# Kernel tuning notes

Measured on AMD Instinct MI355X. Metric: run time of the kernel, lower is better.

The kernel has to match this reference:

```python
import jax, jax.numpy as jnp
import numpy as np

N, E, F_IN, HID, HEADS = 10000, 160000, 70, 256, 4
NEG_SLOPE = 0.2


def setup_inputs() -> dict:
    key = jax.random.key(0)
    ks = jax.random.split(key, 12)
    p = lambda k, shape: jax.random.normal(k, shape, jnp.float32) * 0.05
    return dict(
        node_features=jax.random.normal(ks[0], (N, F_IN), jnp.float32),
        edge_index=jax.random.randint(ks[1], (2, E), 0, N),
        edge_attr=jax.random.normal(ks[2], (E, 4), jnp.float32),
        W1=p(ks[3], (F_IN, HEADS * HID)),
        att_src1=p(ks[4], (HEADS, HID)),
        att_dst1=p(ks[5], (HEADS, HID)),
        b1=jnp.zeros((HEADS * HID,), jnp.float32),
        W2=p(ks[6], (HEADS * HID, HID)),
        att_src2=p(ks[7], (1, HID)),
        att_dst2=p(ks[8], (1, HID)),
        b2=jnp.zeros((HID,), jnp.float32),
        Wv1=p(ks[9], (HID, 128)),
        bv1=jnp.zeros((128,), jnp.float32),
        Wv2=p(ks[10], (128, 1)),
        bv2=jnp.zeros((1,), jnp.float32),
    )


def _gat_layer(x, src, dst, W, a_src, a_dst, b, heads, ch, concat):
    """PyG GATConv (edge_dim=None, add_self_loops already applied to src/dst)."""
    n = x.shape[0]
    h = (x @ W).reshape(n, heads, ch)                      # [N,H,C]
    a_s = (h * a_src).sum(-1)                              # [N,H]
    a_d = (h * a_dst).sum(-1)                              # [N,H]
    e = jax.nn.leaky_relu(a_s[src] + a_d[dst], NEG_SLOPE)  # [E,H]
    # segment softmax over incoming edges of each destination node
    m = jax.ops.segment_max(e, dst, num_segments=n)        # [N,H]
    m = jnp.where(jnp.isfinite(m), m, 0.0)
    ex = jnp.exp(e - m[dst])
    denom = jax.ops.segment_sum(ex, dst, num_segments=n)[dst] + 1e-16
    alpha = ex / denom                                     # [E,H]
    out = jax.ops.segment_sum(h[src] * alpha[..., None], dst, num_segments=n)  # [N,H,C]
    out = out.reshape(n, heads * ch) if concat else out.mean(axis=1)
    return out + b


def reference(node_features, edge_index, edge_attr, W1, att_src1, att_dst1, b1,
              W2, att_src2, att_dst2, b2, Wv1, bv1, Wv2, bv2):
    # edge_attr is ignored: GATConv built without edge_dim has lin_edge=None.
    n = node_features.shape[0]
    loops = jnp.arange(n, dtype=edge_index.dtype)
    src = jnp.concatenate([edge_index[0], loops])
    dst = jnp.concatenate([edge_index[1], loops])
    x = jax.nn.relu(_gat_layer(node_features, src, dst, W1, att_src1, att_dst1, b1, HEADS, HID, True))
    x = jax.nn.relu(_gat_layer(x, src, dst, W2, att_src2, att_dst2, b2, 1, HID, False))
    pooled = x.mean(axis=0, keepdims=True)                 # [1,HID]
    hmid = jax.nn.gelu(pooled @ Wv1 + bv1, approximate=False)
    return hmid @ Wv2 + bv2                                # [1,1]
```

## Files before the change

### kernel.cpp

```cpp
#include <hip/hip_runtime.h>
#include <math.h>

#define NN   10000
#define NE   160000
#define NET  (NE + NN)
#define FIN  70
#define HIDC 256
#define NH   4
#define D1   1024
#define SLOPE 0.2f
#define KL1  96
#define NPB  32
#define BCAP 64

typedef float f32x4 __attribute__((ext_vector_type(4)));
typedef short bf16x8 __attribute__((ext_vector_type(8)));
typedef unsigned short u16x4 __attribute__((ext_vector_type(4)));

__device__ __forceinline__ unsigned short f32_to_bf16(float f) {
    unsigned int u = __float_as_uint(f);
    unsigned int r = u + 0x7fffu + ((u >> 16) & 1u);
    return (unsigned short)(r >> 16);
}
__device__ __forceinline__ float bf16_to_f32(unsigned short h) {
    return __uint_as_float(((unsigned int)h) << 16);
}
__device__ __forceinline__ float leaky(float e) { return (e > 0.f) ? e : SLOPE * e; }

__device__ __forceinline__ void cp16(const unsigned short* g, unsigned short* l) {
    __builtin_amdgcn_global_load_lds((const __attribute__((address_space(1))) unsigned int*)g,
                                     (__attribute__((address_space(3))) unsigned int*)l,
                                     16, 0, 0);
}

__global__ __launch_bounds__(256) void k_prep(const float* __restrict__ W2,
                                              unsigned short* __restrict__ W2t,
                                              const float* __restrict__ W1,
                                              unsigned short* __restrict__ W1t,
                                              const float* __restrict__ asrc,
                                              const float* __restrict__ adst,
                                              const float* __restrict__ x,
                                              unsigned short* __restrict__ xb,
                                              const int* __restrict__ ei,
                                              int* __restrict__ cnt,
                                              int* __restrict__ ssrc,
                                              float* __restrict__ asn,
                                              float* __restrict__ adn) {
    __shared__ __align__(16) char smem[20480];
    int b = blockIdx.x, t = threadIdx.x;
    int lane = t & 63, wave = t >> 6;
    if (b < 64) {
        unsigned short (*tl)[68] = (unsigned short (*)[68])smem;
        int kk0 = (b >> 2) * 64, n0 = (b & 3) * 64;
        for (int i = t; i < 64 * 64; i += 256) {
            int nl = i & 63, kl = i >> 6;
            tl[nl][kl] = f32_to_bf16(W2[(size_t)(kk0 + kl) * HIDC + n0 + nl]);
        }
        __syncthreads();
        for (int i = t; i < 64 * 64; i += 256) {
            int kl = i & 63, nl = i >> 6;
            W2t[(size_t)(n0 + nl) * 1024 + kk0 + kl] = tl[nl][kl];
        }
    } else if (b < 80) {
        unsigned short (*tl)[97] = (unsigned short (*)[97])smem;
        int r0 = (b - 64) * 64;
        for (int i = t; i < 64 * 96; i += 256) {
            int rl = i & 63, kk = i >> 6;
            float w = (kk < FIN) ? W1[(size_t)kk * D1 + r0 + rl] : 0.f;
            tl[rl][kk] = f32_to_bf16(w);
        }
        __syncthreads();
        for (int i = t; i < 64 * 96; i += 256) {
            int kk = i % 96, rl = i / 96;
            W1t[(size_t)(r0 + rl) * KL1 + kk] = tl[rl][kk];
        }
    } else if (b < 120) {
        size_t base = (size_t)(b - 80) * 17500;
        for (int v = t; v < 4375; v += 256) {
            float4 xv = *(const float4*)&x[base + v * 4];
            u16x4 o;
            o[0] = f32_to_bf16(xv.x); o[1] = f32_to_bf16(xv.y);
            o[2] = f32_to_bf16(xv.z); o[3] = f32_to_bf16(xv.w);
            *(u16x4*)&xb[base + v * 4] = o;
        }
    } else if (b < 785) {
        int e = (b - 120) * 256 + t;
        if (e < NET) {
            int src, dst;
            if (e < NE) { src = ei[e]; dst = ei[NE + e]; }
            else        { src = e - NE; dst = src; }
            int pos = atomicAdd(&cnt[dst], 1);
            if (pos < BCAP) ssrc[dst * BCAP + pos] = src;
        }
    } else {
        int n0 = (b - 785) * 64;
        float (*xs)[71] = (float (*)[71])smem;
        float* lws = (float*)(smem + 64 * 71 * 4);
        float* lwd = lws + NH * FIN;
        for (int i = t; i < 64 * FIN; i += 256) {
            int r = i / FIN, k = i % FIN;
            int n = n0 + r;
            xs[r][k] = (n < NN) ? x[(size_t)n * FIN + k] : 0.f;
        }
        float ar[16], dr[16];
#pragma unroll
        for (int q = 0; q < 4; q++) {
            float4 av = *(const float4*)&asrc[lane * 16 + q * 4];
            float4 dv = *(const float4*)&adst[lane * 16 + q * 4];
            ar[q*4+0]=av.x; ar[q*4+1]=av.y; ar[q*4+2]=av.z; ar[q*4+3]=av.w;
            dr[q*4+0]=dv.x; dr[q*4+1]=dv.y; dr[q*4+2]=dv.z; dr[q*4+3]=dv.w;
        }
        for (int k = wave; k < FIN; k += 4) {
            const float* row = W1 + (size_t)k * D1 + lane * 16;
            float s = 0.f, dd = 0.f;
#pragma unroll
            for (int q = 0; q < 4; q++) {
                float4 wv = *(const float4*)(row + q * 4);
                s  += wv.x*ar[q*4] + wv.y*ar[q*4+1] + wv.z*ar[q*4+2] + wv.w*ar[q*4+3];
                dd += wv.x*dr[q*4] + wv.y*dr[q*4+1] + wv.z*dr[q*4+2] + wv.w*dr[q*4+3];
            }
#pragma unroll
            for (int off = 1; off < 16; off <<= 1) { s += __shfl_xor(s, off); dd += __shfl_xor(dd, off); }
            if ((lane & 15) == 0) { int h = lane >> 4; lws[h * FIN + k] = s; lwd[h * FIN + k] = dd; }
        }
        __syncthreads();
        if (t < 64) {
            int n = n0 + t;
            if (n < NN) {
                float a[NH] = {}, d2[NH] = {};
                for (int k = 0; k < FIN; k++) {
                    float xv = xs[t][k];
#pragma unroll
                    for (int h = 0; h < NH; h++) {
                        a[h]  += xv * lws[h * FIN + k];
                        d2[h] += xv * lwd[h * FIN + k];
                    }
                }
#pragma unroll
                for (int h = 0; h < NH; h++) { asn[n*NH+h] = a[h]; adn[n*NH+h] = d2[h]; }
            }
        }
    }
}

__global__ __launch_bounds__(256) void k_sm_aggX(const int* __restrict__ cnt,
                                                 const int* __restrict__ ssrc,
                                                 const float* __restrict__ as,
                                                 const float* __restrict__ ad,
                                                 const unsigned short* __restrict__ xb,
                                                 unsigned short* __restrict__ aggXhi) {
    int t = threadIdx.x, lane = t & 63, wave = t >> 6;
    int d = blockIdx.x * 4 + wave;
    int n = cnt[d]; if (n > BCAP) n = BCAP;
    float4 adv = *(const float4*)&ad[d * NH];
    bool v0 = lane < n;
    int s0 = 0;
    float e0[NH];
    if (v0) {
        s0 = ssrc[d * BCAP + lane];
        float4 a4 = *(const float4*)&as[s0 * NH];
        e0[0] = leaky(a4.x + adv.x); e0[1] = leaky(a4.y + adv.y);
        e0[2] = leaky(a4.z + adv.z); e0[3] = leaky(a4.w + adv.w);
    } else { e0[0] = e0[1] = e0[2] = e0[3] = -1e30f; }
    float m[NH] = {e0[0], e0[1], e0[2], e0[3]};
#pragma unroll
    for (int h = 0; h < NH; h++)
        for (int off = 32; off > 0; off >>= 1)
            m[h] = fmaxf(m[h], __shfl_xor(m[h], off));
    float sum[NH];
#pragma unroll
    for (int h = 0; h < NH; h++) sum[h] = v0 ? expf(e0[h] - m[h]) : 0.f;
#pragma unroll
    for (int h = 0; h < NH; h++)
        for (int off = 32; off > 0; off >>= 1)
            sum[h] += __shfl_xor(sum[h], off);
    __shared__ float al4[4][64][4];
    __shared__ int   sid[4][64];
    if (v0) {
        sid[wave][lane] = s0;
#pragma unroll
        for (int h = 0; h < NH; h++) al4[wave][lane][h] = expf(e0[h] - m[h]) / (sum[h] + 1e-16f);
    }
    __syncthreads();
    float ac[NH][2] = {};
#pragma unroll 4
    for (int j = 0; j < n; j++) {
        int s = sid[wave][j];
        float4 al = *(const float4*)al4[wave][j];
        float xv0 = bf16_to_f32(xb[(size_t)s * FIN + lane]);
        float xv1 = (lane < FIN - 64) ? bf16_to_f32(xb[(size_t)s * FIN + 64 + lane]) : 0.f;
        ac[0][0] += al.x * xv0; ac[0][1] += al.x * xv1;
        ac[1][0] += al.y * xv0; ac[1][1] += al.y * xv1;
        ac[2][0] += al.z * xv0; ac[2][1] += al.z * xv1;
        ac[3][0] += al.w * xv0; ac[3][1] += al.w * xv1;
    }
#pragma unroll
    for (int h = 0; h < NH; h++) {
        size_t base = ((size_t)d * NH + h) * KL1;
        aggXhi[base + lane] = f32_to_bf16(ac[h][0]);
        if (lane < 32) {
            float v1 = (lane < FIN - 64) ? ac[h][1] : 0.f;
            aggXhi[base + 64 + lane] = f32_to_bf16(v1);
        }
    }
}

__global__ __launch_bounds__(256) void k_gemm_l1(const unsigned short* __restrict__ aggXhi,
                                                 const unsigned short* __restrict__ W1t,
                                                 const float* __restrict__ b1,
                                                 unsigned short* __restrict__ x2hi) {
    __shared__ unsigned short As[128 * 96];
    __shared__ unsigned short Bs[128 * 96];
    int t = threadIdx.x;
    int n0 = blockIdx.x * 128;
    int cb = blockIdx.y * 128;
    int h  = blockIdx.z;
    int lane = t & 63, wave = t >> 6, quad = lane >> 4, l16 = lane & 15;
    int wr = (wave & 1) * 64, wc = (wave >> 1) * 64;
#pragma unroll
    for (int q = 0; q < 6; q++) {
        int g = q * 256 + t;
        int row = g / 12, gr = g % 12;
        int ra = n0 + row; if (ra >= NN) ra = NN - 1;
        cp16(aggXhi + ((size_t)ra * NH + h) * KL1 + gr * 8, As + g * 8);
        cp16(W1t + (size_t)(h * 256 + cb + row) * KL1 + gr * 8, Bs + g * 8);
    }
    __syncthreads();
    f32x4 acc[4][4] = {};
#pragma unroll
    for (int kc = 0; kc < 3; kc++) {
        bf16x8 af[4], bf[4];
#pragma unroll
        for (int i = 0; i < 4; i++) af[i] = *(const bf16x8*)&As[(wr + i * 16 + l16) * KL1 + kc * 32 + quad * 8];
#pragma unroll
        for (int j = 0; j < 4; j++) bf[j] = *(const bf16x8*)&Bs[(wc + j * 16 + l16) * KL1 + kc * 32 + quad * 8];
#pragma unroll
        for (int i = 0; i < 4; i++)
#pragma unroll
            for (int j = 0; j < 4; j++)
                acc[i][j] = __builtin_amdgcn_mfma_f32_16x16x32_bf16(af[i], bf[j], acc[i][j], 0, 0, 0);
    }
#pragma unroll
    for (int i = 0; i < 4; i++)
#pragma unroll
        for (int j = 0; j < 4; j++) {
            int colg = h * 256 + cb + wc + j * 16 + l16;
            float bb = b1[colg];
#pragma unroll
            for (int reg = 0; reg < 4; reg++) {
                int r = n0 + wr + i * 16 + quad * 4 + reg;
                if (r >= NN) continue;
                float v = fmaxf(acc[i][j][reg] + bb, 0.f);
                x2hi[(size_t)r * D1 + colg] = f32_to_bf16(v);
            }
        }
}

__global__ __launch_bounds__(256) void k_gemm2(const unsigned short* __restrict__ x2hi,
                                               const unsigned short* __restrict__ W2t,
                                               const float* __restrict__ asrc,
                                               const float* __restrict__ adst,
                                               unsigned short* __restrict__ h2bf,
                                               float* __restrict__ as2,
                                               float* __restrict__ ad2) {
    __shared__ unsigned short As[64 * 128];
    __shared__ unsigned short Bs[64 * 128];
    int t = threadIdx.x;
    int n0 = blockIdx.x * 64;
    int cb = blockIdx.y * 64;
    int lane = t & 63, wave = t >> 6, quad = lane >> 4, l16 = lane & 15;
    int wr = (wave & 1) * 32, wc = (wave >> 1) * 32;
    const unsigned short* ga[4];
    unsigned short* la[4];
    const unsigned short* gb[4];
    unsigned short* lb[4];
#pragma unroll
    for (int q = 0; q < 4; q++) {
        int g = q * 256 + t;
        int row = g >> 4, gr = g & 15;
        int ra = n0 + row; if (ra >= NN) ra = NN - 1;
        ga[q] = x2hi + (size_t)ra * D1 + gr * 8;
        la[q] = As + g * 8;
        gb[q] = W2t + (size_t)(cb + row) * 1024 + gr * 8;
        lb[q] = Bs + g * 8;
    }
    f32x4 acc[2][2] = {};
    for (int kc = 0; kc < 8; kc++) {
#pragma unroll
        for (int q = 0; q < 4; q++) {
            cp16(ga[q] + kc * 128, la[q]);
            cp16(gb[q] + kc * 128, lb[q]);
        }
        __syncthreads();
#pragma unroll
        for (int ks = 0; ks < 4; ks++) {
            bf16x8 af[2], bf[2];
#pragma unroll
            for (int i = 0; i < 2; i++) af[i] = *(const bf16x8*)&As[(wr + i * 16 + l16) * 128 + ks * 32 + quad * 8];
#pragma unroll
            for (int j = 0; j < 2; j++) bf[j] = *(const bf16x8*)&Bs[(wc + j * 16 + l16) * 128 + ks * 32 + quad * 8];
#pragma unroll
            for (int i = 0; i < 2; i++)
#pragma unroll
                for (int j = 0; j < 2; j++)
                    acc[i][j] = __builtin_amdgcn_mfma_f32_16x16x32_bf16(af[i], bf[j], acc[i][j], 0, 0, 0);
        }
        __syncthreads();
    }
    float a2[2], d2[2];
#pragma unroll
    for (int j = 0; j < 2; j++) {
        int c = cb + wc + j * 16 + l16;
        a2[j] = asrc[c];
        d2[j] = adst[c];
    }
    float asp[2][4] = {}, adp[2][4] = {};
#pragma unroll
    for (int i = 0; i < 2; i++)
#pragma unroll
        for (int j = 0; j < 2; j++) {
            int c = cb + wc + j * 16 + l16;
#pragma unroll
            for (int reg = 0; reg < 4; reg++) {
                int r = n0 + wr + i * 16 + quad * 4 + reg;
                float v = acc[i][j][reg];
                if (r < NN) h2bf[(size_t)r * HIDC + c] = f32_to_bf16(v);
                asp[i][reg] += v * a2[j];
                adp[i][reg] += v * d2[j];
            }
        }
#pragma unroll
    for (int mask = 1; mask < 16; mask <<= 1)
#pragma unroll
        for (int i = 0; i < 2; i++)
#pragma unroll
            for (int reg = 0; reg < 4; reg++) {
                asp[i][reg] += __shfl_xor(asp[i][reg], mask);
                adp[i][reg] += __shfl_xor(adp[i][reg], mask);
            }
    if (l16 == 0) {
#pragma unroll
        for (int i = 0; i < 2; i++)
#pragma unroll
            for (int reg = 0; reg < 4; reg++) {
                int r = n0 + wr + i * 16 + quad * 4 + reg;
                if (r < NN) {
                    atomicAdd(&as2[r], asp[i][reg]);
                    atomicAdd(&ad2[r], adp[i][reg]);
                }
            }
    }
}

__global__ __launch_bounds__(256) void k_sm_aggr2(const int* __restrict__ cnt,
                                                  const int* __restrict__ ssrc,
                                                  const float* __restrict__ as,
                                                  const float* __restrict__ ad,
                                                  const unsigned short* __restrict__ h2bf,
                                                  const float* __restrict__ b,
                                                  float* __restrict__ pooled32) {
    int t = threadIdx.x, lane = t & 63, wave = t >> 6;
    int d = blockIdx.x * 4 + wave;
    int n = cnt[d]; if (n > BCAP) n = BCAP;
    float adv = ad[d];
    bool v0 = lane < n;
    int s0 = v0 ? ssrc[d * BCAP + lane] : 0;
    float e0 = v0 ? leaky(as[s0] + adv) : -1e30f;
    float m = e0;
    for (int off = 32; off > 0; off >>= 1) m = fmaxf(m, __shfl_xor(m, off));
    float ex = v0 ? expf(e0 - m) : 0.f;
    float sum = ex;
    for (int off = 32; off > 0; off >>= 1) sum += __shfl_xor(sum, off);
    float al0 = ex * (1.0f / (sum + 1e-16f));
    float a0 = 0.f, a1 = 0.f, a2v = 0.f, a3 = 0.f;
#pragma unroll 4
    for (int j = 0; j < n; j++) {
        float alj = __shfl(al0, j);
        int   sj  = __shfl(s0, j);
        u16x4 hv = *(const u16x4*)&h2bf[(size_t)sj * HIDC + lane * 4];
        a0  += alj * bf16_to_f32(hv[0]);
        a1  += alj * bf16_to_f32(hv[1]);
        a2v += alj * bf16_to_f32(hv[2]);
        a3  += alj * bf16_to_f32(hv[3]);
    }
    float4 bb = *(const float4*)&b[lane * 4];
    __shared__ float sacc[4 * 256];
    *(float4*)&sacc[wave * 256 + lane * 4] = make_float4(fmaxf(a0 + bb.x, 0.f),
                                                         fmaxf(a1 + bb.y, 0.f),
                                                         fmaxf(a2v + bb.z, 0.f),
                                                         fmaxf(a3 + bb.w, 0.f));
    __syncthreads();
    float s = sacc[t] + sacc[256 + t] + sacc[512 + t] + sacc[768 + t];
    atomicAdd(&pooled32[(blockIdx.x & (NPB - 1)) * HIDC + t], s);
}

__global__ __launch_bounds__(128) void k_mlp(const float* __restrict__ pooled32,
                                             const float* __restrict__ Wv1,
                                             const float* __restrict__ bv1,
                                             const float* __restrict__ Wv2,
                                             const float* __restrict__ bv2,
                                             float* __restrict__ out) {
    int j = threadIdx.x;
    __shared__ float ps[256];
    for (int c = j; c < HIDC; c += 128) {
        float s = 0.f;
        for (int bkt = 0; bkt < NPB; bkt++) s += pooled32[bkt * HIDC + c];
        ps[c] = s;
    }
    __syncthreads();
    float s = bv1[j];
    const float invn = 1.0f / (float)NN;
    for (int c = 0; c < HIDC; c++)
        s += (ps[c] * invn) * Wv1[c * 128 + j];
    float g = 0.5f * s * (1.0f + erff(s * 0.70710678118654752f));
    float v = g * Wv2[j];
    __shared__ float red[128];
    red[j] = v;
    __syncthreads();
    for (int off = 64; off > 0; off >>= 1) {
        if (j < off) red[j] += red[j + off];
        __syncthreads();
    }
    if (j == 0) out[0] = red[0] + bv2[0];
}

extern "C" void kernel_launch(void* const* d_in, const int* in_sizes, int n_in,
                              void* d_out, int out_size, void* d_ws, size_t ws_size,
                              hipStream_t stream) {
    const float* x_in  = (const float*)d_in[0];
    const int*   ei    = (const int*)d_in[1];
    const float* W1    = (const float*)d_in[3];
    const float* asrc1 = (const float*)d_in[4];
    const float* adst1 = (const float*)d_in[5];
    const float* b1    = (const float*)d_in[6];
    const float* W2    = (const float*)d_in[7];
    const float* asrc2 = (const float*)d_in[8];
    const float* adst2 = (const float*)d_in[9];
    const float* b2    = (const float*)d_in[10];
    const float* Wv1   = (const float*)d_in[11];
    const float* bv1   = (const float*)d_in[12];
    const float* Wv2   = (const float*)d_in[13];
    const float* bv2   = (const float*)d_in[14];
    float* out = (float*)d_out;

    char* w = (char*)d_ws;
    auto alloc = [&](size_t bytes) { char* p = w; w += (bytes + 255) & ~(size_t)255; return p; };
    unsigned short* x2hi   = (unsigned short*)alloc(2ull * NN * D1);
    unsigned short* aggXhi = (unsigned short*)alloc(2ull * NN * NH * KL1);
    unsigned short* h2bf = (unsigned short*)alloc(2ull * NN * HIDC);
    unsigned short* xb   = (unsigned short*)alloc(2ull * NN * FIN);
    unsigned short* W2t  = (unsigned short*)alloc(2ull * 256 * 1024);
    unsigned short* W1t  = (unsigned short*)alloc(2ull * NH * 256 * KL1);
    float* as1    = (float*)alloc(sizeof(float) * NN * NH);
    float* ad1    = (float*)alloc(sizeof(float) * NN * NH);
    int*   ssrc   = (int*)alloc(sizeof(int) * NN * BCAP);
    size_t zbytes = (size_t)NN * 4 + NPB * HIDC * 4 + NN * 4 + NN * 4;
    char*  zbase  = alloc(zbytes);
    int*   cnt      = (int*)zbase;
    float* pooled32 = (float*)(zbase + NN * 4);
    float* as2      = (float*)(zbase + NN * 4 + NPB * HIDC * 4);
    float* ad2      = (float*)(zbase + NN * 4 + NPB * HIDC * 4 + NN * 4);

    hipMemsetAsync(zbase, 0, zbytes, stream);

    k_prep<<<64 + 16 + 40 + 665 + 157, 256, 0, stream>>>(
        W2, W2t, W1, W1t, asrc1, adst1, x_in, xb, ei, cnt, ssrc, as1, ad1);

    k_sm_aggX<<<NN / 4, 256, 0, stream>>>(cnt, ssrc, as1, ad1, xb, aggXhi);
    {
        dim3 g((NN + 127) / 128, 2, NH);
        k_gemm_l1<<<g, 256, 0, stream>>>(aggXhi, W1t, b1, x2hi);
    }

    {
        dim3 g((NN + 63) / 64, 4);
        k_gemm2<<<g, 256, 0, stream>>>(x2hi, W2t, asrc2, adst2, h2bf, as2, ad2);
    }

    k_sm_aggr2<<<NN / 4, 256, 0, stream>>>(cnt, ssrc, as2, ad2, h2bf, b2, pooled32);

    k_mlp<<<1, 128, 0, stream>>>(pooled32, Wv1, bv1, Wv2, bv2, out);
}
```

Baseline: 207.8 us.

## Fuse layer-1 GEMM and layer-2 GEMM into one kernel keeping x2 in LDS

Merges the layer-1 projection GEMM (aggX times W1 with bias and ReLU) and the layer-2 GEMM (x2 times W2 with attention dot products) into one kernel that processes 32 nodes per block. The intermediate 1024-wide x2 activation stays in LDS with an XOR swizzle instead of a 20MB bf16 round trip through global memory. It also removes one launch. In exchange, W1 and W2 fragments are read straight from global or L2 per block with no LDS staging, and there are only 313 blocks with small 32-row tiles, which may hurt occupancy and the MFMA feed rate.

```diff
diff --git a/kernel.cpp b/kernel.cpp
--- a/kernel.cpp
+++ b/kernel.cpp
@@ -26,12 +26,6 @@
     return __uint_as_float(((unsigned int)h) << 16);
 }
 __device__ __forceinline__ float leaky(float e) { return (e > 0.f) ? e : SLOPE * e; }
-
-__device__ __forceinline__ void cp16(const unsigned short* g, unsigned short* l) {
-    __builtin_amdgcn_global_load_lds((const __attribute__((address_space(1))) unsigned int*)g,
-                                     (__attribute__((address_space(3))) unsigned int*)l,
-                                     16, 0, 0);
-}
 
 __global__ __launch_bounds__(256) void k_prep(const float* __restrict__ W2,
                                               unsigned short* __restrict__ W2t,
@@ -205,112 +199,91 @@
     }
 }
 
-__global__ __launch_bounds__(256) void k_gemm_l1(const unsigned short* __restrict__ aggXhi,
-                                                 const unsigned short* __restrict__ W1t,
-                                                 const float* __restrict__ b1,
-                                                 unsigned short* __restrict__ x2hi) {
-    __shared__ unsigned short As[128 * 96];
-    __shared__ unsigned short Bs[128 * 96];
+__global__ __launch_bounds__(256) void k_gemm12(const unsigned short* __restrict__ aggXhi,
+                                                const unsigned short* __restrict__ W1t,
+                                                const float* __restrict__ b1,
+                                                const unsigned short* __restrict__ W2t,
+                                                const float* __restrict__ asrc,
+                                                const float* __restrict__ adst,
+                                                unsigned short* __restrict__ h2bf,
+                                                float* __restrict__ as2,
+                                                float* __restrict__ ad2) {
+    __shared__ unsigned short aggXs[32 * 392];
+    __shared__ unsigned short x2s[32 * 512];
     int t = threadIdx.x;
-    int n0 = blockIdx.x * 128;
-    int cb = blockIdx.y * 128;
-    int h  = blockIdx.z;
+    int n0 = blockIdx.x * 32;
     int lane = t & 63, wave = t >> 6, quad = lane >> 4, l16 = lane & 15;
-    int wr = (wave & 1) * 64, wc = (wave >> 1) * 64;
 #pragma unroll
     for (int q = 0; q < 6; q++) {
         int g = q * 256 + t;
-        int row = g / 12, gr = g % 12;
-        int ra = n0 + row; if (ra >= NN) ra = NN - 1;
-        cp16(aggXhi + ((size_t)ra * NH + h) * KL1 + gr * 8, As + g * 8);
-        cp16(W1t + (size_t)(h * 256 + cb + row) * KL1 + gr * 8, Bs + g * 8);
+        int node = g / 48, gr = g % 48;
+        int ra = n0 + node; if (ra >= NN) ra = NN - 1;
+        float4 v = *(const float4*)(aggXhi + (size_t)ra * 384 + gr * 8);
+        *(float4*)&aggXs[node * 392 + gr * 8] = v;
     }
     __syncthreads();
-    f32x4 acc[4][4] = {};
-#pragma unroll
-    for (int kc = 0; kc < 3; kc++) {
-        bf16x8 af[4], bf[4];
-#pragma unroll
-        for (int i = 0; i < 4; i++) af[i] = *(const bf16x8*)&As[(wr + i * 16 + l16) * KL1 + kc * 32 + quad * 8];
-#pragma unroll
-        for (int j = 0; j < 4; j++) bf[j] = *(const bf16x8*)&Bs[(wc + j * 16 + l16) * KL1 + kc * 32 + quad * 8];
-#pragma unroll
-        for (int i = 0; i < 4; i++)
-#pragma unroll
-            for (int j = 0; j < 4; j++)
-                acc[i][j] = __builtin_amdgcn_mfma_f32_16x16x32_bf16(af[i], bf[j], acc[i][j], 0, 0, 0);
-    }
-#pragma unroll
-    for (int i = 0; i < 4; i++)
-#pragma unroll
-        for (int j = 0; j < 4; j++) {
-            int colg = h * 256 + cb + wc + j * 16 + l16;
-            float bb = b1[colg];
-#pragma unroll
-            for (int reg = 0; reg < 4; reg++) {
-                int r = n0 + wr + i * 16 + quad * 4 + reg;
-                if (r >= NN) continue;
-                float v = fmaxf(acc[i][j][reg] + bb, 0.f);
-                x2hi[(size_t)r * D1 + colg] = f32_to_bf16(v);
-            }
-        }
-}
-
-__global__ __launch_bounds__(256) void k_gemm2(const unsigned short* __restrict__ x2hi,
-                                               const unsigned short* __restrict__ W2t,
-                                               const float* __restrict__ asrc,
-                                               const float* __restrict__ adst,
-                                               unsigned short* __restrict__ h2bf,
-                                               float* __restrict__ as2,
-                                               float* __restrict__ ad2) {
-    __shared__ unsigned short As[64 * 128];
-    __shared__ unsigned short Bs[64 * 128];
-    int t = threadIdx.x;
-    int n0 = blockIdx.x * 64;
-    int cb = blockIdx.y * 64;
-    int lane = t & 63, wave = t >> 6, quad = lane >> 4, l16 = lane & 15;
-    int wr = (wave & 1) * 32, wc = (wave >> 1) * 32;
-    const unsigned short* ga[4];
-    unsigned short* la[4];
-    const unsigned short* gb[4];
-    unsigned short* lb[4];
-#pragma unroll
-    for (int q = 0; q < 4; q++) {
-        int g = q * 256 + t;
-        int row = g >> 4, gr = g & 15;
-        int ra = n0 + row; if (ra >= NN) ra = NN - 1;
-        ga[q] = x2hi + (size_t)ra * D1 + gr * 8;
-        la[q] = As + g * 8;
-        gb[q] = W2t + (size_t)(cb + row) * 1024 + gr * 8;
-        lb[q] = Bs + g * 8;
-    }
-    f32x4 acc[2][2] = {};
-    for (int kc = 0; kc < 8; kc++) {
-#pragma unroll
-        for (int q = 0; q < 4; q++) {
-            cp16(ga[q] + kc * 128, la[q]);
-            cp16(gb[q] + kc * 128, lb[q]);
-        }
+    f32x4 acc2[2][4] = {};
+    for (int ko = 0; ko < 2; ko++) {
+        if (ko) __syncthreads();
+        int h = ko * 2 + (wave >> 1);
+        f32x4 acc1[2][8] = {};
+#pragma unroll
+        for (int kc = 0; kc < 3; kc++) {
+            bf16x8 af[2], bf[8];
+#pragma unroll
+            for (int i = 0; i < 2; i++)
+                af[i] = *(const bf16x8*)&aggXs[(i * 16 + l16) * 392 + h * 96 + kc * 32 + quad * 8];
+#pragma unroll
+            for (int j = 0; j < 8; j++) {
+                int cg = ko * 512 + wave * 128 + j * 16 + l16;
+                bf[j] = *(const bf16x8*)&W1t[(size_t)cg * KL1 + kc * 32 + quad * 8];
+            }
+#pragma unroll
+            for (int i = 0; i < 2; i++)
+#pragma unroll
+                for (int j = 0; j < 8; j++)
+                    acc1[i][j] = __builtin_amdgcn_mfma_f32_16x16x32_bf16(af[i], bf[j], acc1[i][j], 0, 0, 0);
+        }
+#pragma unroll
+        for (int i = 0; i < 2; i++)
+#pragma unroll
+            for (int j = 0; j < 8; j++) {
+                int cl = wave * 128 + j * 16 + l16;
+                float bb = b1[ko * 512 + cl];
+#pragma unroll
+                for (int reg = 0; reg < 4; reg++) {
+                    int lr = i * 16 + quad * 4 + reg;
+                    float v = fmaxf(acc1[i][j][reg] + bb, 0.f);
+                    int sw = (((cl >> 3) ^ (lr & 7)) << 3) | (cl & 7);
+                    x2s[lr * 512 + sw] = f32_to_bf16(v);
+                }
+            }
         __syncthreads();
-#pragma unroll
-        for (int ks = 0; ks < 4; ks++) {
-            bf16x8 af[2], bf[2];
-#pragma unroll
-            for (int i = 0; i < 2; i++) af[i] = *(const bf16x8*)&As[(wr + i * 16 + l16) * 128 + ks * 32 + quad * 8];
-#pragma unroll
-            for (int j = 0; j < 2; j++) bf[j] = *(const bf16x8*)&Bs[(wc + j * 16 + l16) * 128 + ks * 32 + quad * 8];
+#pragma unroll 4
+        for (int ks = 0; ks < 16; ks++) {
+            bf16x8 af[2], bf[4];
+#pragma unroll
+            for (int i = 0; i < 2; i++) {
+                int rr = i * 16 + l16;
+                int gsw = ((ks * 4 + quad) ^ (rr & 7)) << 3;
+                af[i] = *(const bf16x8*)&x2s[rr * 512 + gsw];
+            }
+#pragma unroll
+            for (int j = 0; j < 4; j++) {
+                int c = wave * 64 + j * 16 + l16;
+                bf[j] = *(const bf16x8*)&W2t[(size_t)c * 1024 + ko * 512 + ks * 32 + quad * 8];
+            }
 #pragma unroll
             for (int i = 0; i < 2; i++)
 #pragma unroll
-                for (int j = 0; j < 2; j++)
-                    acc[i][j] = __builtin_amdgcn_mfma_f32_16x16x32_bf16(af[i], bf[j], acc[i][j], 0, 0, 0);
-        }
-        __syncthreads();
-    }
-    float a2[2], d2[2];
-#pragma unroll
-    for (int j = 0; j < 2; j++) {
-        int c = cb + wc + j * 16 + l16;
+                for (int j = 0; j < 4; j++)
+                    acc2[i][j] = __builtin_amdgcn_mfma_f32_16x16x32_bf16(af[i], bf[j], acc2[i][j], 0, 0, 0);
+        }
+    }
+    float a2[4], d2[4];
+#pragma unroll
+    for (int j = 0; j < 4; j++) {
+        int c = wave * 64 + j * 16 + l16;
         a2[j] = asrc[c];
         d2[j] = adst[c];
     }
@@ -318,12 +291,12 @@
 #pragma unroll
     for (int i = 0; i < 2; i++)
 #pragma unroll
-        for (int j = 0; j < 2; j++) {
-            int c = cb + wc + j * 16 + l16;
+        for (int j = 0; j < 4; j++) {
+            int c = wave * 64 + j * 16 + l16;
 #pragma unroll
             for (int reg = 0; reg < 4; reg++) {
-                int r = n0 + wr + i * 16 + quad * 4 + reg;
-                float v = acc[i][j][reg];
+                int r = n0 + i * 16 + quad * 4 + reg;
+                float v = acc2[i][j][reg];
                 if (r < NN) h2bf[(size_t)r * HIDC + c] = f32_to_bf16(v);
                 asp[i][reg] += v * a2[j];
                 adp[i][reg] += v * d2[j];
@@ -343,7 +316,7 @@
         for (int i = 0; i < 2; i++)
 #pragma unroll
             for (int reg = 0; reg < 4; reg++) {
-                int r = n0 + wr + i * 16 + quad * 4 + reg;
+                int r = n0 + i * 16 + quad * 4 + reg;
                 if (r < NN) {
                     atomicAdd(&as2[r], asp[i][reg]);
                     atomicAdd(&ad2[r], adp[i][reg]);
@@ -445,7 +418,6 @@
 
     char* w = (char*)d_ws;
     auto alloc = [&](size_t bytes) { char* p = w; w += (bytes + 255) & ~(size_t)255; return p; };
-    unsigned short* x2hi   = (unsigned short*)alloc(2ull * NN * D1);
     unsigned short* aggXhi = (unsigned short*)alloc(2ull * NN * NH * KL1);
     unsigned short* h2bf = (unsigned short*)alloc(2ull * NN * HIDC);
     unsigned short* xb   = (unsigned short*)alloc(2ull * NN * FIN);
@@ -467,15 +439,9 @@
         W2, W2t, W1, W1t, asrc1, adst1, x_in, xb, ei, cnt, ssrc, as1, ad1);
 
     k_sm_aggX<<<NN / 4, 256, 0, stream>>>(cnt, ssrc, as1, ad1, xb, aggXhi);
-    {
-        dim3 g((NN + 127) / 128, 2, NH);
-        k_gemm_l1<<<g, 256, 0, stream>>>(aggXhi, W1t, b1, x2hi);
-    }
-
-    {
-        dim3 g((NN + 63) / 64, 4);
-        k_gemm2<<<g, 256, 0, stream>>>(x2hi, W2t, asrc2, adst2, h2bf, as2, ad2);
-    }
+
+    k_gemm12<<<(NN + 31) / 32, 256, 0, stream>>>(aggXhi, W1t, b1, W2t, asrc2, adst2,
+                                                 h2bf, as2, ad2);
 
     k_sm_aggr2<<<NN / 4, 256, 0, stream>>>(cnt, ssrc, as2, ad2, h2bf, b2, pooled32);
 
```

Result: slower. 221.0 us (+6.3%).
